# Optimization experiments

Hardware: AMD Instinct MI355X
Metric: run time of the kernel (lower is better)

The kernel has to match this reference:

```python
import jax, jax.numpy as jnp
import numpy as np

B, N = 4096, 128
STATE_DIM, GOAL_DIM, OBSTACLE_DIM = 6, 6, 4
VEH = 2 * STATE_DIM + GOAL_DIM  # 18


def setup_inputs() -> dict:
    key = jax.random.key(0)
    ks = jax.random.split(key, 8)
    s = lambda k, shp, fan: jax.random.normal(k, shp, jnp.float32) / np.sqrt(fan)
    return {
        "obs": jax.random.normal(ks[0], (B, 138), jnp.float32),
        "obstacles": jax.random.uniform(ks[1], (B, 5, N), jnp.float32),
        "act": jax.random.normal(ks[2], (B, 2), jnp.float32),
        "ow1": s(ks[3], (22, 256), 22),
        "ob1": jnp.zeros((256,), jnp.float32),
        "ow2": s(ks[4], (256, 256), 256),
        "ob2": jnp.zeros((256,), jnp.float32),
        "qw1": s(ks[5], (396, 256), 396),
        "qb1": jnp.zeros((256,), jnp.float32),
        "qw2": s(ks[6], (256, 256), 256),
        "qb2": jnp.zeros((256,), jnp.float32),
        "qw3": s(ks[7], (256, 1), 256),
        "qb3": jnp.zeros((1,), jnp.float32),
    }


def reference(obs, obstacles, act, ow1, ob1, ow2, ob2, qw1, qb1, qw2, qb2, qw3, qb3):
    # obs: [B, 138]; obstacles: [B, obstacle_dim+1, N]; act: [B, 2]
    veh = obs[:, :VEH]                                 # [B, 18]
    obst_data = obstacles[:, :OBSTACLE_DIM, :]         # [B, 4, N]
    mask = obstacles[:, -1, :]                         # [B, N]
    # per-obstacle features: concat broadcast vehicle state with obstacle data -> [B, N, 22]
    x = jnp.concatenate(
        [jnp.broadcast_to(veh[:, None, :], (veh.shape[0], obst_data.shape[2], VEH)),
         obst_data.transpose(0, 2, 1)], axis=-1)
    # shared obstacle MLP (ReLU on both layers, incl. output_activation)
    h = jax.nn.relu(jnp.einsum("bnf,fh->bnh", x, ow1) + ob1)
    h = jax.nn.relu(jnp.einsum("bnh,hk->bnk", h, ow2) + ob2)  # [B, N, 256]
    # masked sum-pool over obstacle axis
    pooled = jnp.einsum("bnh,bn->bh", h, mask)         # [B, 256]
    comb = jnp.concatenate([obs, pooled, act], axis=-1)  # [B, 396]
    q = jax.nn.relu(comb @ qw1 + qb1)
    q = jax.nn.relu(q @ qw2 + qb2)
    q = q @ qw3 + qb3                                   # [B, 1]
    return jnp.squeeze(q, -1)
```

## Files before the change

kernel.cpp:

```cpp
#include <hip/hip_runtime.h>
#include <hip/hip_bf16.h>


typedef __attribute__((ext_vector_type(8))) short short8;
typedef __attribute__((ext_vector_type(4))) float f32x4;

#define MFMA16(A, B, C) __builtin_amdgcn_mfma_f32_16x16x32_bf16(A, B, C, 0, 0, 0)

__device__ __forceinline__ unsigned short f2b(float f) {
  __hip_bfloat16 h = __float2bfloat16(f);
  return __builtin_bit_cast(unsigned short, h);
}
__device__ __forceinline__ float b2f(unsigned short u) {
  unsigned v = ((unsigned)u) << 16;
  return __builtin_bit_cast(float, v);
}
__device__ __forceinline__ unsigned pk2(float a, float b) {
  return (unsigned)f2b(a) | ((unsigned)f2b(b) << 16);
}
__device__ __forceinline__ unsigned pk2f(float a, float b) {
  unsigned ua = __builtin_bit_cast(unsigned, a) + 0x8000u;
  unsigned ub = __builtin_bit_cast(unsigned, b) + 0x8000u;
  return __builtin_amdgcn_perm(ub, ua, 0x07060302u);
}

__global__ __launch_bounds__(256) void pack_weights(
    const float* __restrict__ ow1, const float* __restrict__ ow2,
    const float* __restrict__ qw1, const float* __restrict__ qw2,
    unsigned short* __restrict__ ow1q, unsigned short* __restrict__ ow2p,
    unsigned short* __restrict__ qw1h, unsigned short* __restrict__ qw1l,
    unsigned short* __restrict__ qw2h, unsigned short* __restrict__ qw2l) {
  int i = blockIdx.x * 256 + threadIdx.x;
  if (i < 8192) {
    int j = i & 7;
    int l15 = (i >> 3) & 15;
    int quad = (i >> 7) & 3;
    int mt = (i >> 9) & 15;
    int k = quad * 8 + j;
    float v = (k < 22) ? ow1[k * 256 + (mt * 16 + l15)] : 0.f;
    ow1q[i] = f2b(v);
  }
  if (i < 65536) {
    int j = i & 7;
    int n = (i >> 3) & 255;
    int qq = i >> 11;
    int k = (qq >> 2) * 32 + (qq & 3) * 8 + j;
    ow2p[i] = f2b(ow2[k * 256 + n]);
    float w = qw2[k * 256 + n];
    unsigned short h = f2b(w);
    qw2h[i] = h;
    qw2l[i] = f2b(w - b2f(h));
  }
  if (i < 106496) {
    int j = i & 7;
    int n = (i >> 3) & 255;
    int qq = i >> 11;
    int k = (qq >> 2) * 32 + (qq & 3) * 8 + j;
    float w = (k < 396) ? qw1[k * 256 + n] : 0.f;
    unsigned short h = f2b(w);
    qw1h[i] = h;
    qw1l[i] = f2b(w - b2f(h));
  }
}

#define XSTR 40
#define HSTR 264

__global__ __launch_bounds__(256, 2) void obstacle_kernel(
    const float* __restrict__ obs, const float* __restrict__ obstacles,
    const unsigned short* __restrict__ ow1q,
    const unsigned short* __restrict__ ow2p,
    const float* __restrict__ ob1, const float* __restrict__ ob2,
    unsigned short* __restrict__ poolH, unsigned short* __restrict__ poolL) {
  __shared__ unsigned short xs[128 * XSTR];
  __shared__ unsigned short h1[128 * HSTR];
  __shared__ float maskS[128];
  __shared__ unsigned short vehB[32];

  const int b = blockIdx.x;
  const int tid = threadIdx.x;

  if (tid < 18) vehB[tid] = f2b(obs[b * 138 + tid]);
  if (tid < 128) maskS[tid] = obstacles[b * 640 + 512 + tid];
  __syncthreads();

  {
    int n = tid >> 1;
    int half = tid & 1;
    unsigned short* wr = &xs[n * XSTR + half * 16];
    if (half == 0) {
      unsigned short r01[16];
#pragma unroll
      for (int k = 0; k < 16; k++) r01[k] = vehB[k];
      *(short8*)(wr + 0) = *(short8*)&r01[0];
      *(short8*)(wr + 8) = *(short8*)&r01[8];
    } else {
      unsigned short r2[8];
      r2[0] = vehB[16];
      r2[1] = vehB[17];
#pragma unroll
      for (int d = 0; d < 4; d++)
        r2[2 + d] = f2b(obstacles[b * 640 + d * 128 + n]);
      r2[6] = 0; r2[7] = 0;
      *(short8*)(wr + 0) = *(short8*)&r2[0];
      short8 z = {0, 0, 0, 0, 0, 0, 0, 0};
      *(short8*)(wr + 8) = z;
    }
  }
  __syncthreads();

  const int wave = tid >> 6;
  const int lane = tid & 63;
  const int quad = lane >> 4;
  const int l15 = lane & 15;

  {
    const unsigned short* wp = &ow1q[wave * 2048 + quad * 128 + l15 * 8];
    short8 wfr[4];
#pragma unroll
    for (int i = 0; i < 4; i++) wfr[i] = *(const short8*)(wp + i * 512);

    const unsigned short* bxp = &xs[l15 * XSTR + quad * 8];
    short8 bx[8];
#pragma unroll
    for (int nt = 0; nt < 8; nt++)
      bx[nt] = *(const short8*)(bxp + nt * 16 * XSTR);

    const f32x4* bini = (const f32x4*)&ob1[wave * 64 + quad * 4];
    unsigned short* wr = &h1[l15 * HSTR + wave * 64 + quad * 4];

#pragma unroll
    for (int i = 0; i < 4; i++) {
      f32x4 cinit = bini[i * 4];
      f32x4 acc1[8];
#pragma unroll
      for (int nt = 0; nt < 8; nt++) acc1[nt] = MFMA16(wfr[i], bx[nt], cinit);
#pragma unroll
      for (int nt = 0; nt < 8; nt++) {
        float v0 = fmaxf(acc1[nt][0], 0.f);
        float v1 = fmaxf(acc1[nt][1], 0.f);
        float v2 = fmaxf(acc1[nt][2], 0.f);
        float v3 = fmaxf(acc1[nt][3], 0.f);
        uint2 pk;
        pk.x = pk2f(v0, v1);
        pk.y = pk2f(v2, v3);
        *(uint2*)(wr + nt * 16 * HSTR + i * 16) = pk;
      }
    }
  }
  __syncthreads();

  f32x4 acc[8][4];
#pragma unroll
  for (int t = 0; t < 4; t++) {
    float bv = ob2[wave * 64 + t * 16 + l15];
    f32x4 bvec = {bv, bv, bv, bv};
#pragma unroll
    for (int mt = 0; mt < 8; mt++) acc[mt][t] = bvec;
  }

  const unsigned short* bp = &ow2p[(quad * 256 + wave * 64 + l15) * 8];
  const unsigned short* h1r = &h1[l15 * HSTR + quad * 8];
  short8 bcur[4], bnxt[4];
#pragma unroll
  for (int t = 0; t < 4; t++) bcur[t] = *(const short8*)(bp + t * 128);

#pragma unroll 1
  for (int kb = 0; kb < 8; kb++) {
    if (kb < 7) {
#pragma unroll
      for (int t = 0; t < 4; t++)
        bnxt[t] = *(const short8*)(bp + 8192 + t * 128);
    }
    short8 afr[8];
#pragma unroll
    for (int mt = 0; mt < 8; mt++)
      afr[mt] = *(const short8*)(h1r + mt * 16 * HSTR);
#pragma unroll
    for (int mt = 0; mt < 8; mt++)
#pragma unroll
      for (int t = 0; t < 4; t++) acc[mt][t] = MFMA16(afr[mt], bcur[t], acc[mt][t]);
    bp += 8192;
    h1r += 32;
    if (kb < 7) {
#pragma unroll
      for (int t = 0; t < 4; t++) bcur[t] = bnxt[t];
    }
  }

  f32x4 mk[8];
  const float* mkp = &maskS[quad * 4];
#pragma unroll
  for (int mt = 0; mt < 8; mt++) mk[mt] = *(const f32x4*)(mkp + mt * 16);

#pragma unroll
  for (int t = 0; t < 4; t++) {
    float s = 0.f;
#pragma unroll
    for (int mt = 0; mt < 8; mt++) {
#pragma unroll
      for (int r = 0; r < 4; r++) {
        float v = fmaxf(acc[mt][t][r], 0.f);
        s = fmaf(mk[mt][r], v, s);
      }
    }
    s += __shfl_xor(s, 16);
    s += __shfl_xor(s, 32);
    if (quad == 0) {
      int n = wave * 64 + t * 16 + l15;
      unsigned short sh = (unsigned short)(__builtin_bit_cast(unsigned, s) >> 16);
      poolH[b * 256 + n] = sh;
      poolL[b * 256 + n] = f2b(s - b2f(sh));
    }
  }
}

__global__ __launch_bounds__(512) void head_mfma(
    const float* __restrict__ obs, const float* __restrict__ act,
    const unsigned short* __restrict__ poolH,
    const unsigned short* __restrict__ poolL,
    const unsigned short* __restrict__ qw1h,
    const unsigned short* __restrict__ qw1l,
    const unsigned short* __restrict__ qw2h,
    const unsigned short* __restrict__ qw2l,
    const float* __restrict__ qb1, const float* __restrict__ qb2,
    const float* __restrict__ qw3, const float* __restrict__ qb3,
    float* __restrict__ out) {
  const int CSTR = 424;
  const int HSTRQ = 264;
  __shared__ unsigned short combH[16 * 424], combL[16 * 424];
  __shared__ unsigned short h1H[16 * 264], h1L[16 * 264];
  __shared__ float wred[8][16];

  const int tid = threadIdx.x;
  const int r0 = blockIdx.x * 16;

  for (int idx = tid; idx < 16 * 416; idx += 512) {
    int m = idx / 416;
    int k = idx - m * 416;
    unsigned short hi, lo;
    if (k < 138) {
      float v = obs[(r0 + m) * 138 + k];
      hi = f2b(v);
      lo = f2b(v - b2f(hi));
    } else if (k < 394) {
      hi = poolH[(r0 + m) * 256 + (k - 138)];
      lo = poolL[(r0 + m) * 256 + (k - 138)];
    } else if (k < 396) {
      float v = act[(r0 + m) * 2 + (k - 394)];
      hi = f2b(v);
      lo = f2b(v - b2f(hi));
    } else {
      hi = 0; lo = 0;
    }
    combH[m * CSTR + k] = hi;
    combL[m * CSTR + k] = lo;
  }
  __syncthreads();

  const int wave = tid >> 6;
  const int lane = tid & 63;
  const int quad = lane >> 4;
  const int l15 = lane & 15;

  f32x4 acc[2], accm[2];
  acc[0] = acc[1] = accm[0] = accm[1] = (f32x4){0.f, 0.f, 0.f, 0.f};
#pragma unroll 1
  for (int kb = 0; kb < 13; kb++) {
    int ao = l15 * CSTR + kb * 32 + quad * 8;
    short8 ah = *(const short8*)&combH[ao];
    short8 al = *(const short8*)&combL[ao];
#pragma unroll
    for (int t = 0; t < 2; t++) {
      int n = (wave * 2 + t) * 16 + l15;
      int off = ((kb * 4 + quad) * 256 + n) * 8;
      short8 bh = *(const short8*)&qw1h[off];
      short8 bl = *(const short8*)&qw1l[off];
      acc[t] = MFMA16(ah, bh, acc[t]);
      accm[t] = MFMA16(ah, bl, accm[t]);
      accm[t] = MFMA16(al, bh, accm[t]);
    }
  }
#pragma unroll
  for (int t = 0; t < 2; t++) {
    int n = (wave * 2 + t) * 16 + l15;
    float bias = qb1[n];
#pragma unroll
    for (int r = 0; r < 4; r++) {
      int m = quad * 4 + r;
      float v = fmaxf(acc[t][r] + accm[t][r] + bias, 0.f);
      unsigned short hi = f2b(v);
      h1H[m * HSTRQ + n] = hi;
      h1L[m * HSTRQ + n] = f2b(v - b2f(hi));
    }
  }
  __syncthreads();

  f32x4 a2[2], a2m[2];
  a2[0] = a2[1] = a2m[0] = a2m[1] = (f32x4){0.f, 0.f, 0.f, 0.f};
#pragma unroll 1
  for (int kb = 0; kb < 8; kb++) {
    int ao = l15 * HSTRQ + kb * 32 + quad * 8;
    short8 ah = *(const short8*)&h1H[ao];
    short8 al = *(const short8*)&h1L[ao];
#pragma unroll
    for (int t = 0; t < 2; t++) {
      int n = (wave * 2 + t) * 16 + l15;
      int off = ((kb * 4 + quad) * 256 + n) * 8;
      short8 bh = *(const short8*)&qw2h[off];
      short8 bl = *(const short8*)&qw2l[off];
      a2[t] = MFMA16(ah, bh, a2[t]);
      a2m[t] = MFMA16(ah, bl, a2m[t]);
      a2m[t] = MFMA16(al, bh, a2m[t]);
    }
  }

#pragma unroll
  for (int r = 0; r < 4; r++) {
    float s = 0.f;
#pragma unroll
    for (int t = 0; t < 2; t++) {
      int n = (wave * 2 + t) * 16 + l15;
      float v = fmaxf(a2[t][r] + a2m[t][r] + qb2[n], 0.f);
      s += v * qw3[n];
    }
    s += __shfl_xor(s, 1);
    s += __shfl_xor(s, 2);
    s += __shfl_xor(s, 4);
    s += __shfl_xor(s, 8);
    if (l15 == 0) wred[wave][quad * 4 + r] = s;
  }
  __syncthreads();
  if (tid < 16) {
    float s = qb3[0];
#pragma unroll
    for (int w = 0; w < 8; w++) s += wred[w][tid];
    out[r0 + tid] = s;
  }
}

extern "C" void kernel_launch(void* const* d_in, const int* in_sizes, int n_in,
                              void* d_out, int out_size, void* d_ws, size_t ws_size,
                              hipStream_t stream) {
  const float* obs       = (const float*)d_in[0];
  const float* obstacles = (const float*)d_in[1];
  const float* act       = (const float*)d_in[2];
  const float* ow1       = (const float*)d_in[3];
  const float* ob1       = (const float*)d_in[4];
  const float* ow2       = (const float*)d_in[5];
  const float* ob2       = (const float*)d_in[6];
  const float* qw1       = (const float*)d_in[7];
  const float* qb1       = (const float*)d_in[8];
  const float* qw2       = (const float*)d_in[9];
  const float* qb2       = (const float*)d_in[10];
  const float* qw3       = (const float*)d_in[11];
  const float* qb3       = (const float*)d_in[12];
  float* out = (float*)d_out;

  unsigned short* ow1q = (unsigned short*)d_ws;
  unsigned short* ow2p = ow1q + 8192;
  unsigned short* qw1h = ow2p + 65536;
  unsigned short* qw1l = qw1h + 106496;
  unsigned short* qw2h = qw1l + 106496;
  unsigned short* qw2l = qw2h + 65536;
  unsigned short* poolH = qw2l + 65536;
  unsigned short* poolL = poolH + 1048576;

  pack_weights<<<416, 256, 0, stream>>>(ow1, ow2, qw1, qw2, ow1q, ow2p, qw1h,
                                        qw1l, qw2h, qw2l);
  obstacle_kernel<<<4096, 256, 0, stream>>>(obs, obstacles, ow1q, ow2p, ob1,
                                            ob2, poolH, poolL);
  head_mfma<<<256, 512, 0, stream>>>(obs, act, poolH, poolL, qw1h, qw1l, qw2h,
                                     qw2l, qb1, qb2, qw3, qb3, out);
}
```

Measured before the change: 176.6 us.

## Split obstacle pooling across two blocks per batch row and widen head blocks

Each batch row's 128 obstacles are now handled by two blocks of 64, so twice as many blocks run and each uses half the LDS and accumulator registers; launch bounds are raised to 4 blocks per CU. The two partial pooled sums go out as fp32 and are added and split into hi/lo bf16 in the head kernel. The head kernel doubles to 1024 threads with one output tile per wave. The trade-off is that every block reloads the full ow2 weights, and the partial buffer doubles global traffic for the pooled sums.

```diff
diff --git a/kernel.cpp b/kernel.cpp
--- a/kernel.cpp
+++ b/kernel.cpp
@@ -14,9 +14,6 @@
 __device__ __forceinline__ float b2f(unsigned short u) {
   unsigned v = ((unsigned)u) << 16;
   return __builtin_bit_cast(float, v);
-}
-__device__ __forceinline__ unsigned pk2(float a, float b) {
-  return (unsigned)f2b(a) | ((unsigned)f2b(b) << 16);
 }
 __device__ __forceinline__ unsigned pk2f(float a, float b) {
   unsigned ua = __builtin_bit_cast(unsigned, a) + 0x8000u;
@@ -66,25 +63,27 @@
 #define XSTR 40
 #define HSTR 264
 
-__global__ __launch_bounds__(256, 2) void obstacle_kernel(
+__global__ __launch_bounds__(256, 4) void obstacle_kernel(
     const float* __restrict__ obs, const float* __restrict__ obstacles,
     const unsigned short* __restrict__ ow1q,
     const unsigned short* __restrict__ ow2p,
     const float* __restrict__ ob1, const float* __restrict__ ob2,
-    unsigned short* __restrict__ poolH, unsigned short* __restrict__ poolL) {
-  __shared__ unsigned short xs[128 * XSTR];
-  __shared__ unsigned short h1[128 * HSTR];
-  __shared__ float maskS[128];
+    float* __restrict__ part) {
+  __shared__ unsigned short xs[64 * XSTR];
+  __shared__ unsigned short h1[64 * HSTR];
+  __shared__ float maskS[64];
   __shared__ unsigned short vehB[32];
 
-  const int b = blockIdx.x;
+  const int b2 = blockIdx.x;
+  const int bb = b2 >> 1;
+  const int r0 = (b2 & 1) * 64;
   const int tid = threadIdx.x;
 
-  if (tid < 18) vehB[tid] = f2b(obs[b * 138 + tid]);
-  if (tid < 128) maskS[tid] = obstacles[b * 640 + 512 + tid];
-  __syncthreads();
-
-  {
+  if (tid < 18) vehB[tid] = f2b(obs[bb * 138 + tid]);
+  if (tid < 64) maskS[tid] = obstacles[bb * 640 + 512 + r0 + tid];
+  __syncthreads();
+
+  if (tid < 128) {
     int n = tid >> 1;
     int half = tid & 1;
     unsigned short* wr = &xs[n * XSTR + half * 16];
@@ -100,7 +99,7 @@
       r2[1] = vehB[17];
 #pragma unroll
       for (int d = 0; d < 4; d++)
-        r2[2 + d] = f2b(obstacles[b * 640 + d * 128 + n]);
+        r2[2 + d] = f2b(obstacles[bb * 640 + d * 128 + r0 + n]);
       r2[6] = 0; r2[7] = 0;
       *(short8*)(wr + 0) = *(short8*)&r2[0];
       short8 z = {0, 0, 0, 0, 0, 0, 0, 0};
@@ -121,9 +120,9 @@
     for (int i = 0; i < 4; i++) wfr[i] = *(const short8*)(wp + i * 512);
 
     const unsigned short* bxp = &xs[l15 * XSTR + quad * 8];
-    short8 bx[8];
-#pragma unroll
-    for (int nt = 0; nt < 8; nt++)
+    short8 bx[4];
+#pragma unroll
+    for (int nt = 0; nt < 4; nt++)
       bx[nt] = *(const short8*)(bxp + nt * 16 * XSTR);
 
     const f32x4* bini = (const f32x4*)&ob1[wave * 64 + quad * 4];
@@ -132,11 +131,11 @@
 #pragma unroll
     for (int i = 0; i < 4; i++) {
       f32x4 cinit = bini[i * 4];
-      f32x4 acc1[8];
-#pragma unroll
-      for (int nt = 0; nt < 8; nt++) acc1[nt] = MFMA16(wfr[i], bx[nt], cinit);
-#pragma unroll
-      for (int nt = 0; nt < 8; nt++) {
+      f32x4 acc1[4];
+#pragma unroll
+      for (int nt = 0; nt < 4; nt++) acc1[nt] = MFMA16(wfr[i], bx[nt], cinit);
+#pragma unroll
+      for (int nt = 0; nt < 4; nt++) {
         float v0 = fmaxf(acc1[nt][0], 0.f);
         float v1 = fmaxf(acc1[nt][1], 0.f);
         float v2 = fmaxf(acc1[nt][2], 0.f);
@@ -150,13 +149,13 @@
   }
   __syncthreads();
 
-  f32x4 acc[8][4];
+  f32x4 acc[4][4];
 #pragma unroll
   for (int t = 0; t < 4; t++) {
     float bv = ob2[wave * 64 + t * 16 + l15];
     f32x4 bvec = {bv, bv, bv, bv};
 #pragma unroll
-    for (int mt = 0; mt < 8; mt++) acc[mt][t] = bvec;
+    for (int mt = 0; mt < 4; mt++) acc[mt][t] = bvec;
   }
 
   const unsigned short* bp = &ow2p[(quad * 256 + wave * 64 + l15) * 8];
@@ -172,12 +171,12 @@
       for (int t = 0; t < 4; t++)
         bnxt[t] = *(const short8*)(bp + 8192 + t * 128);
     }
-    short8 afr[8];
-#pragma unroll
-    for (int mt = 0; mt < 8; mt++)
+    short8 afr[4];
+#pragma unroll
+    for (int mt = 0; mt < 4; mt++)
       afr[mt] = *(const short8*)(h1r + mt * 16 * HSTR);
 #pragma unroll
-    for (int mt = 0; mt < 8; mt++)
+    for (int mt = 0; mt < 4; mt++)
 #pragma unroll
       for (int t = 0; t < 4; t++) acc[mt][t] = MFMA16(afr[mt], bcur[t], acc[mt][t]);
     bp += 8192;
@@ -188,16 +187,16 @@
     }
   }
 
-  f32x4 mk[8];
+  f32x4 mk[4];
   const float* mkp = &maskS[quad * 4];
 #pragma unroll
-  for (int mt = 0; mt < 8; mt++) mk[mt] = *(const f32x4*)(mkp + mt * 16);
+  for (int mt = 0; mt < 4; mt++) mk[mt] = *(const f32x4*)(mkp + mt * 16);
 
 #pragma unroll
   for (int t = 0; t < 4; t++) {
     float s = 0.f;
 #pragma unroll
-    for (int mt = 0; mt < 8; mt++) {
+    for (int mt = 0; mt < 4; mt++) {
 #pragma unroll
       for (int r = 0; r < 4; r++) {
         float v = fmaxf(acc[mt][t][r], 0.f);
@@ -206,19 +205,13 @@
     }
     s += __shfl_xor(s, 16);
     s += __shfl_xor(s, 32);
-    if (quad == 0) {
-      int n = wave * 64 + t * 16 + l15;
-      unsigned short sh = (unsigned short)(__builtin_bit_cast(unsigned, s) >> 16);
-      poolH[b * 256 + n] = sh;
-      poolL[b * 256 + n] = f2b(s - b2f(sh));
-    }
-  }
-}
-
-__global__ __launch_bounds__(512) void head_mfma(
+    if (quad == 0) part[b2 * 256 + wave * 64 + t * 16 + l15] = s;
+  }
+}
+
+__global__ __launch_bounds__(1024) void head_mfma(
     const float* __restrict__ obs, const float* __restrict__ act,
-    const unsigned short* __restrict__ poolH,
-    const unsigned short* __restrict__ poolL,
+    const float* __restrict__ part,
     const unsigned short* __restrict__ qw1h,
     const unsigned short* __restrict__ qw1l,
     const unsigned short* __restrict__ qw2h,
@@ -230,12 +223,12 @@
   const int HSTRQ = 264;
   __shared__ unsigned short combH[16 * 424], combL[16 * 424];
   __shared__ unsigned short h1H[16 * 264], h1L[16 * 264];
-  __shared__ float wred[8][16];
+  __shared__ float wred[16][16];
 
   const int tid = threadIdx.x;
   const int r0 = blockIdx.x * 16;
 
-  for (int idx = tid; idx < 16 * 416; idx += 512) {
+  for (int idx = tid; idx < 16 * 416; idx += 1024) {
     int m = idx / 416;
     int k = idx - m * 416;
     unsigned short hi, lo;
@@ -244,8 +237,10 @@
       hi = f2b(v);
       lo = f2b(v - b2f(hi));
     } else if (k < 394) {
-      hi = poolH[(r0 + m) * 256 + (k - 138)];
-      lo = poolL[(r0 + m) * 256 + (k - 138)];
+      int g = (r0 + m) * 2;
+      float v = part[g * 256 + (k - 138)] + part[(g + 1) * 256 + (k - 138)];
+      hi = f2b(v);
+      lo = f2b(v - b2f(hi));
     } else if (k < 396) {
       float v = act[(r0 + m) * 2 + (k - 394)];
       hi = f2b(v);
@@ -262,33 +257,27 @@
   const int lane = tid & 63;
   const int quad = lane >> 4;
   const int l15 = lane & 15;
-
-  f32x4 acc[2], accm[2];
-  acc[0] = acc[1] = accm[0] = accm[1] = (f32x4){0.f, 0.f, 0.f, 0.f};
+  const int n = wave * 16 + l15;
+
+  f32x4 acc = {0.f, 0.f, 0.f, 0.f}, accm = {0.f, 0.f, 0.f, 0.f};
 #pragma unroll 1
   for (int kb = 0; kb < 13; kb++) {
     int ao = l15 * CSTR + kb * 32 + quad * 8;
     short8 ah = *(const short8*)&combH[ao];
     short8 al = *(const short8*)&combL[ao];
-#pragma unroll
-    for (int t = 0; t < 2; t++) {
-      int n = (wave * 2 + t) * 16 + l15;
-      int off = ((kb * 4 + quad) * 256 + n) * 8;
-      short8 bh = *(const short8*)&qw1h[off];
-      short8 bl = *(const short8*)&qw1l[off];
-      acc[t] = MFMA16(ah, bh, acc[t]);
-      accm[t] = MFMA16(ah, bl, accm[t]);
-      accm[t] = MFMA16(al, bh, accm[t]);
-    }
-  }
-#pragma unroll
-  for (int t = 0; t < 2; t++) {
-    int n = (wave * 2 + t) * 16 + l15;
+    int off = ((kb * 4 + quad) * 256 + n) * 8;
+    short8 bh = *(const short8*)&qw1h[off];
+    short8 bl = *(const short8*)&qw1l[off];
+    acc = MFMA16(ah, bh, acc);
+    accm = MFMA16(ah, bl, accm);
+    accm = MFMA16(al, bh, accm);
+  }
+  {
     float bias = qb1[n];
 #pragma unroll
     for (int r = 0; r < 4; r++) {
       int m = quad * 4 + r;
-      float v = fmaxf(acc[t][r] + accm[t][r] + bias, 0.f);
+      float v = fmaxf(acc[r] + accm[r] + bias, 0.f);
       unsigned short hi = f2b(v);
       h1H[m * HSTRQ + n] = hi;
       h1L[m * HSTRQ + n] = f2b(v - b2f(hi));
@@ -296,45 +285,39 @@
   }
   __syncthreads();
 
-  f32x4 a2[2], a2m[2];
-  a2[0] = a2[1] = a2m[0] = a2m[1] = (f32x4){0.f, 0.f, 0.f, 0.f};
+  f32x4 a2 = {0.f, 0.f, 0.f, 0.f}, a2m = {0.f, 0.f, 0.f, 0.f};
 #pragma unroll 1
   for (int kb = 0; kb < 8; kb++) {
     int ao = l15 * HSTRQ + kb * 32 + quad * 8;
     short8 ah = *(const short8*)&h1H[ao];
     short8 al = *(const short8*)&h1L[ao];
-#pragma unroll
-    for (int t = 0; t < 2; t++) {
-      int n = (wave * 2 + t) * 16 + l15;
-      int off = ((kb * 4 + quad) * 256 + n) * 8;
-      short8 bh = *(const short8*)&qw2h[off];
-      short8 bl = *(const short8*)&qw2l[off];
-      a2[t] = MFMA16(ah, bh, a2[t]);
-      a2m[t] = MFMA16(ah, bl, a2m[t]);
-      a2m[t] = MFMA16(al, bh, a2m[t]);
-    }
-  }
-
-#pragma unroll
-  for (int r = 0; r < 4; r++) {
-    float s = 0.f;
-#pragma unroll
-    for (int t = 0; t < 2; t++) {
-      int n = (wave * 2 + t) * 16 + l15;
-      float v = fmaxf(a2[t][r] + a2m[t][r] + qb2[n], 0.f);
-      s += v * qw3[n];
-    }
-    s += __shfl_xor(s, 1);
-    s += __shfl_xor(s, 2);
-    s += __shfl_xor(s, 4);
-    s += __shfl_xor(s, 8);
-    if (l15 == 0) wred[wave][quad * 4 + r] = s;
+    int off = ((kb * 4 + quad) * 256 + n) * 8;
+    short8 bh = *(const short8*)&qw2h[off];
+    short8 bl = *(const short8*)&qw2l[off];
+    a2 = MFMA16(ah, bh, a2);
+    a2m = MFMA16(ah, bl, a2m);
+    a2m = MFMA16(al, bh, a2m);
+  }
+
+  {
+    float w3 = qw3[n];
+    float qb2n = qb2[n];
+#pragma unroll
+    for (int r = 0; r < 4; r++) {
+      float v = fmaxf(a2[r] + a2m[r] + qb2n, 0.f);
+      float s = v * w3;
+      s += __shfl_xor(s, 1);
+      s += __shfl_xor(s, 2);
+      s += __shfl_xor(s, 4);
+      s += __shfl_xor(s, 8);
+      if (l15 == 0) wred[wave][quad * 4 + r] = s;
+    }
   }
   __syncthreads();
   if (tid < 16) {
     float s = qb3[0];
 #pragma unroll
-    for (int w = 0; w < 8; w++) s += wred[w][tid];
+    for (int w = 0; w < 16; w++) s += wred[w][tid];
     out[r0 + tid] = s;
   }
 }
@@ -363,13 +346,12 @@
   unsigned short* qw1l = qw1h + 106496;
   unsigned short* qw2h = qw1l + 106496;
   unsigned short* qw2l = qw2h + 65536;
-  unsigned short* poolH = qw2l + 65536;
-  unsigned short* poolL = poolH + 1048576;
+  float* part = (float*)(qw2l + 65536);
 
   pack_weights<<<416, 256, 0, stream>>>(ow1, ow2, qw1, qw2, ow1q, ow2p, qw1h,
                                         qw1l, qw2h, qw2l);
-  obstacle_kernel<<<4096, 256, 0, stream>>>(obs, obstacles, ow1q, ow2p, ob1,
-                                            ob2, poolH, poolL);
-  head_mfma<<<256, 512, 0, stream>>>(obs, act, poolH, poolL, qw1h, qw1l, qw2h,
-                                     qw2l, qb1, qb2, qw3, qb3, out);
-}
+  obstacle_kernel<<<8192, 256, 0, stream>>>(obs, obstacles, ow1q, ow2p, ob1,
+                                            ob2, part);
+  head_mfma<<<256, 1024, 0, stream>>>(obs, act, part, qw1h, qw1l, qw2h,
+                                      qw2l, qb1, qb2, qw3, qb3, out);
+}
```

Measured after the change: 171.2 us. 1.03x faster.
